# Kernel tuning notes

Hardware: AMD Instinct MI355X
Metric: run time of the kernel (lower is better)

## Reference

```python
import jax, jax.numpy as jnp
import numpy as np

B, N, D = 8, 1024, 768
H = 3
DCAT = 2 * D          # 1536, input dim at layer 1
DK = DCAT // H        # 512
CONV_OUT = D - 2      # 766 (kernel 3, VALID)


def setup_inputs() -> dict:
    key = jax.random.key(0)
    ks = jax.random.split(key, 20)
    s = 0.02
    return {
        "adj": jax.random.uniform(ks[0], (B, N, N), dtype=jnp.float32),
        "inputs": jax.random.normal(ks[1], (B, N, D), dtype=jnp.float32),
        "score_mask": jax.random.randint(ks[2], (B, H, N, N), 0, 2).astype(bool),
        # GCN layer weights (stored [in,out]; math = torch Linear)
        "W0_w": jax.random.normal(ks[3], (D, D), dtype=jnp.float32) * s,
        "W0_b": jnp.zeros((D,), dtype=jnp.float32),
        "W1_w": jax.random.normal(ks[4], (DCAT, D), dtype=jnp.float32) * s,
        "W1_b": jnp.zeros((D,), dtype=jnp.float32),
        # MultiHeadAttention(3, 1536) query/key projections
        "q_w": jax.random.normal(ks[5], (DCAT, DCAT), dtype=jnp.float32) * s,
        "q_b": jnp.zeros((DCAT,), dtype=jnp.float32),
        "k_w": jax.random.normal(ks[6], (DCAT, DCAT), dtype=jnp.float32) * s,
        "k_b": jnp.zeros((DCAT,), dtype=jnp.float32),
        # Conv1d(n, n, 3) created in forward: OIH layout
        "conv_w": jax.random.normal(ks[7], (N, N, 3), dtype=jnp.float32) * s,
        "conv_b": jnp.zeros((N,), dtype=jnp.float32),
        # linearc: 766 -> 768
        "linc_w": jax.random.normal(ks[8], (CONV_OUT, D), dtype=jnp.float32) * s,
        "linc_b": jnp.zeros((D,), dtype=jnp.float32),
        # fc: Linear(768,768,no bias) -> ReLU -> Linear(768,768,no bias)
        "fc1_w": jax.random.normal(ks[9], (D, D), dtype=jnp.float32) * s,
        "fc2_w": jax.random.normal(ks[10], (D, D), dtype=jnp.float32) * s,
    }


def _gcn_layer(adj, x, denom, Ww, Wb):
    Ax = adj @ x                       # [B,n,din]
    AxW = (Ax @ Ww + Wb) / denom       # [B,n,768]
    return jax.nn.relu(AxW) + (x @ Ww + Wb)


def _select_top2(m):
    # per-batch top-2 threshold over flattened NxN, symmetrize, diag=1
    b, n, _ = m.shape
    flat = m.reshape(b, -1)
    thr = jax.lax.top_k(flat, 2)[0][:, -1]                  # [b]
    mask = (flat >= thr[:, None]).astype(m.dtype).reshape(b, n, n)
    mask = mask + jnp.swapaxes(mask, -1, -2)
    eye = jnp.eye(n, dtype=m.dtype)
    return mask * (1.0 - eye) + eye


def reference(adj, inputs, score_mask, W0_w, W0_b, W1_w, W1_b,
              q_w, q_b, k_w, k_b, conv_w, conv_b, linc_w, linc_b,
              fc1_w, fc2_w):
    b, n, d = inputs.shape
    # ---- layer 0 ----
    denom = adj.sum(2, keepdims=True) + 1.0
    out = _gcn_layer(adj, inputs, denom, W0_w, W0_b)        # [B,n,768]
    # Conv1d over feature axis with channels = n, VALID, k=3 -> [B,n,766]
    conve = jax.nn.relu(
        jax.lax.conv_general_dilated(out, conv_w, (1,), 'VALID',
                                     dimension_numbers=('NCH', 'OIH', 'NCH'))
        + conv_b[None, :, None])
    out = conve @ linc_w + linc_b                           # [B,n,768]
    # ---- layer 1 (semantic path) ----
    x = jnp.concatenate([inputs, out], axis=-1)             # [B,n,1536]
    h, dk = H, x.shape[-1] // H
    q = (x @ q_w + q_b).reshape(b, n, h, dk).transpose(0, 2, 1, 3)
    k = (x @ k_w + k_b).reshape(b, n, h, dk).transpose(0, 2, 1, 3)
    scores = jnp.einsum('bhqd,bhkd->bhqk', q, k) / jnp.sqrt(jnp.float32(dk))
    scores = jnp.where(score_mask, jnp.float32(-1e9), scores)
    keep = (~score_mask[:, :, :, 0:1]).astype(scores.dtype)
    attn = jax.nn.softmax(scores, axis=-1) * keep           # [B,3,n,n]
    # attention-driven head selection (softmax over batch dim, argmax over heads)
    prob = jax.nn.softmax(attn.sum((-2, -1)), axis=0)       # [B,3]
    max_idx = jnp.argmax(prob, axis=1)                      # [B]
    adj2 = jnp.take_along_axis(attn, max_idx[:, None, None, None], axis=1)[:, 0]
    adj2 = _select_top2(adj2) * adj2
    denom2 = adj2.sum(2, keepdims=True) + 1.0
    out = _gcn_layer(adj2, x, denom2, W1_w, W1_b)
    out = jax.nn.relu(out @ fc1_w) @ fc2_w
    return out
```

## Files before the change

### kernel.cpp

```cpp
#include <hip/hip_runtime.h>
#include <cstdint>
#include <cstddef>

typedef __bf16 bf16;
typedef __bf16 bf16x8 __attribute__((ext_vector_type(8)));
typedef float f32x4 __attribute__((ext_vector_type(4)));

#define B_ 8
#define N_ 1024
#define D_ 768
#define H_ 3
#define DC_ 1536
#define DK_ 512
#define PC_ 766
#define MB_ (1024ull*1024ull)

static const size_t O_DEN   = 0;
static const size_t O_DEN2  = 32768;
static const size_t O_ADIAG = 65536;
static const size_t O_T2P   = 98304;
static const size_t O_THR   = 163840;
static const size_t O_CNTS  = 164096;
static const size_t O_HSEL  = 164352;
static const size_t O_SELC  = 164608;
static const size_t O_FLAG  = 164864;
static const size_t O_QKB   = 165120;
static const size_t O_SEL   = 180224;
static const size_t O_ATTN  = 262144;
static const size_t O_X     = O_ATTN + 32*MB_;
static const size_t O_AX2   = O_X    + 24*MB_;
static const size_t O_ADJB  = O_AX2  + 24*MB_;
static const size_t O_INT   = O_ADJB + 16*MB_;
static const size_t O_BBA   = O_INT  + 12*MB_;
static const size_t O_BBB   = O_BBA  + 12*MB_;
static const size_t O_BBC   = O_BBB  + 12*MB_;
static const size_t O_W0T   = O_BBC  + 12*MB_;
static const size_t O_W1T   = O_W0T + 1179648;
static const size_t O_QKWT  = O_W1T + 2359296;
static const size_t O_CWB   = O_QKWT + 9437184;
static const size_t O_LCT   = O_CWB + 6291456;
static const size_t O_F1T   = O_LCT + 1179648;
static const size_t O_F2T   = O_F1T + 1179648;
static const size_t WS_NEED = O_F2T + 1179648;
static const size_t O_OUT0T = O_INT;

__device__ __forceinline__ bool mask_at(const void* p, int flag, size_t i) {
    switch (flag) {
        case 1:  return ((const int*)p)[i] != 0;
        case 2:  return ((const float*)p)[i] != 0.0f;
        case 3:  return ((const long long*)p)[i] != 0;
        default: return ((const unsigned char*)p)[i] != 0;
    }
}

__device__ __forceinline__ void gload16(const void* g, void* l) {
    __builtin_amdgcn_global_load_lds(
        (const __attribute__((address_space(1))) void*)g,
        (__attribute__((address_space(3))) void*)l, 16, 0, 0);
}

__device__ inline float blockMax256(float v) {
    __shared__ float red[4];
    for (int off = 32; off; off >>= 1) v = fmaxf(v, __shfl_xor(v, off));
    int lane = threadIdx.x & 63, wid = threadIdx.x >> 6;
    if (lane == 0) red[wid] = v;
    __syncthreads();
    v = fmaxf(fmaxf(red[0], red[1]), fmaxf(red[2], red[3]));
    __syncthreads();
    return v;
}

__device__ inline float blockSum256(float v) {
    __shared__ float red[4];
    for (int off = 32; off; off >>= 1) v += __shfl_xor(v, off);
    int lane = threadIdx.x & 63, wid = threadIdx.x >> 6;
    if (lane == 0) red[wid] = v;
    __syncthreads();
    v = red[0] + red[1] + red[2] + red[3];
    __syncthreads();
    return v;
}

template<int EPI>
__global__ __launch_bounds__(256) void mm(
    const bf16* __restrict__ A, size_t sA, int lda,
    const bf16* __restrict__ Bt, size_t sB, int ldb,
    const int* __restrict__ rowIdx, int rowMul,
    const float* __restrict__ bias,
    const bf16* __restrict__ Dadd, int ldd,
    const float* __restrict__ denv,
    const void* __restrict__ smask, const int* __restrict__ flagp,
    bf16* __restrict__ Cb, float* __restrict__ Cf, size_t sC, int ldc,
    int M, int N, int K,
    const bf16* __restrict__ Bt2, const float* __restrict__ bias2,
    bf16* __restrict__ Cb2, size_t sC2, int ldc2)
{
    __shared__ __align__(16) bf16 As[2][64 * 64];
    __shared__ __align__(16) bf16 Bs[2][128 * 64];

    const int gx = gridDim.x, gy = gridDim.y;
    const int nwg = gx * gy * (int)gridDim.z;
    int lin = ((int)blockIdx.z * gy + (int)blockIdx.y) * gx + (int)blockIdx.x;
    int cpx = nwg >> 3;
    int swz = (lin & 7) * cpx + (lin >> 3);
    int ty = swz % gy;
    int tt = swz / gy;
    int tx = tt % gx;
    int b  = tt / gx;

    const int bm = ty * 64, bn = tx * 128;
    const int tid = threadIdx.x;
    const int lane = tid & 63, w = tid >> 6;
    const int wr = w >> 1, wc = w & 1;
    const int boff = rowIdx ? rowIdx[b] * rowMul : 0;

    const bf16* Ab = A + (size_t)b * sA;
    const bf16* Bb = Bt + (size_t)b * sB;

    const bf16* Bsrc = Bb;
    int bRow0 = boff + bn;
    if (EPI == 7 && bn >= 1024) { Bsrc = Bt2; bRow0 = bn - 1024; }

    const int sr = lane >> 3;
    const int gk = ((lane & 7) ^ (lane >> 3)) * 8;

    f32x4 zero = {0.f, 0.f, 0.f, 0.f};
    f32x4 acc[2][4];
    #pragma unroll
    for (int i = 0; i < 2; ++i)
        #pragma unroll
        for (int j = 0; j < 4; ++j) acc[i][j] = zero;

    #pragma unroll
    for (int q = 0; q < 2; ++q)
        gload16((const void*)(Ab + (size_t)(bm + w * 16 + q * 8 + sr) * lda + gk),
                (void*)(As[0] + (w * 16 + q * 8) * 64));
    #pragma unroll
    for (int q = 0; q < 4; ++q)
        gload16((const void*)(Bsrc + (size_t)(bRow0 + w * 32 + q * 8 + sr) * ldb + gk),
                (void*)(Bs[0] + (w * 32 + q * 8) * 64));

    const int rl = lane & 15;
    const int g8 = lane >> 4;
    const int rx = lane & 7;

    int cur = 0;
    for (int k0 = 0; k0 < K; k0 += 64) {
        int nxt = cur ^ 1;
        if (k0 + 64 < K) {
            #pragma unroll
            for (int q = 0; q < 2; ++q)
                gload16((const void*)(Ab + (size_t)(bm + w * 16 + q * 8 + sr) * lda + k0 + 64 + gk),
                        (void*)(As[nxt] + (w * 16 + q * 8) * 64));
            #pragma unroll
            for (int q = 0; q < 4; ++q)
                gload16((const void*)(Bsrc + (size_t)(bRow0 + w * 32 + q * 8 + sr) * ldb + k0 + 64 + gk),
                        (void*)(Bs[nxt] + (w * 32 + q * 8) * 64));
            asm volatile("s_waitcnt vmcnt(6)" ::: "memory");
        } else {
            asm volatile("s_waitcnt vmcnt(0)" ::: "memory");
        }
        __builtin_amdgcn_s_barrier();
        __builtin_amdgcn_sched_barrier(0);

        bf16x8 af[2][2], bfv[4][2];
        #pragma unroll
        for (int ks = 0; ks < 2; ++ks) {
            int e = ks * 4 + g8;
            #pragma unroll
            for (int i = 0; i < 2; ++i)
                af[i][ks] = *(const bf16x8*)(As[cur] + (wr * 32 + i * 16 + rl) * 64 + (e ^ rx) * 8);
            #pragma unroll
            for (int j = 0; j < 4; ++j)
                bfv[j][ks] = *(const bf16x8*)(Bs[cur] + (wc * 64 + j * 16 + rl) * 64 + (e ^ rx) * 8);
        }
        #pragma unroll
        for (int ks = 0; ks < 2; ++ks)
            #pragma unroll
            for (int i = 0; i < 2; ++i)
                #pragma unroll
                for (int j = 0; j < 4; ++j)
                    acc[i][j] = __builtin_amdgcn_mfma_f32_16x16x32_bf16(af[i][ks], bfv[j][ks], acc[i][j], 0, 0, 0);

        __builtin_amdgcn_s_barrier();
        __builtin_amdgcn_sched_barrier(0);
        cur = nxt;
    }

    const int r0 = (lane >> 4) * 4, c0 = lane & 15;
    int flag = 0, h0 = 0;
    if (EPI == 4) { flag = flagp[0]; h0 = rowIdx[b]; }
    #pragma unroll
    for (int i = 0; i < 2; ++i) {
        #pragma unroll
        for (int r = 0; r < 4; ++r) {
            int m = bm + wr * 32 + i * 16 + r0 + r;
            #pragma unroll
            for (int j = 0; j < 4; ++j) {
                int n = bn + wc * 64 + j * 16 + c0;
                float v = acc[i][j][r];
                size_t oidx = (size_t)b * sC + (size_t)m * ldc + n;
                if (EPI == 0) {
                    Cb[oidx] = (bf16)(v + bias[boff + n]);
                } else if (EPI == 1) {
                    v = fmaxf((v + bias[n]) / denv[(size_t)b * M + m], 0.f)
                        + (float)Dadd[((size_t)b * M + m) * ldd + n];
                    Cb[oidx] = (bf16)v;
                } else if (EPI == 2) {
                    Cb[oidx] = (bf16)fmaxf(v, 0.f);
                } else if (EPI == 3) {
                    Cf[oidx] = v;
                } else if (EPI == 4) {
                    size_t mi = (((size_t)b * H_ + h0) * N_ + m) * N_ + n;
                    Cf[oidx] = mask_at(smask, flag, mi) ? -1e9f : v * 0.04419417382415922f;
                } else if (EPI == 5) {
                    Cb[oidx] = (n < PC_) ? (bf16)fmaxf(v + bias[m], 0.f) : (bf16)0.f;
                } else if (EPI == 7) {
                    if (n < 1024)
                        Cb[(size_t)b * sC + (size_t)m * ldc + n] = (bf16)(v + bias[boff + n]);
                    else
                        Cb2[(size_t)b * sC2 + (size_t)m * ldc2 + (n - 1024)] = (bf16)(v + bias2[n - 1024]);
                } else {
                    Cb[oidx] = (bf16)v;
                }
            }
        }
    }
}


__device__ int d_detect(const unsigned int* __restrict__ sm) {
    __shared__ int sGt1, sF32, sOddNZ, sFlag;
    if (threadIdx.x == 0) { sGt1 = 0; sF32 = 0; sOddNZ = 0; }
    __syncthreads();
    int gt1 = 0, f32c = 0, oddnz = 0;
    for (int s = 0; s < 16; ++s) {
        int idx = s * 256 + threadIdx.x;
        unsigned wv = sm[idx];
        if (wv > 1u) gt1 = 1;
        if (wv == 0x3F800000u) f32c++;
        if ((idx & 1) && wv != 0u) oddnz = 1;
    }
    if (gt1)   atomicOr(&sGt1, 1);
    if (f32c)  atomicAdd(&sF32, f32c);
    if (oddnz) atomicOr(&sOddNZ, 1);
    __syncthreads();
    if (threadIdx.x == 0) {
        int f;
        if (sF32 > 512) f = 2;
        else if (!sGt1) f = sOddNZ ? 1 : 3;
        else f = 0;
        sFlag = f;
    }
    __syncthreads();
    return sFlag;
}

__device__ void d_trcvt(const float* __restrict__ src, bf16* __restrict__ dst,
                        int R, int C, int Rpad, int Cpad,
                        size_t sSrc, size_t sDst, int mode, int bx, int by, int bz) {
    __shared__ float t[32][33];
    int r0 = by * 32, c0 = bx * 32;
    int tx = threadIdx.x & 31, ty = threadIdx.x >> 5;
    const float* s = src + (size_t)bz * sSrc;
    bf16* d = dst + (size_t)bz * sDst;
    #pragma unroll
    for (int q = 0; q < 4; ++q) {
        int r = r0 + ty + q * 8, c = c0 + tx;
        t[ty + q * 8][tx] = (r < R && c < C) ? s[(size_t)r * C + c] : 0.f;
    }
    __syncthreads();
    #pragma unroll
    for (int q = 0; q < 4; ++q) {
        int dr = c0 + ty + q * 8, dc = r0 + tx;
        if (dr < Cpad && dc < Rpad) {
            int drm = dr;
            if (mode == 1) drm = (dr >> 9) * 1024 + (dr & 511);
            else if (mode == 2) drm = (dr >> 9) * 1024 + 512 + (dr & 511);
            d[(size_t)drm * Rpad + dc] = (bf16)t[tx][ty + q * 8];
        }
    }
}

#define PB_DET   1
#define PB_QKB   13
#define PB_CW2   1037
#define PB_ADJ   9229
#define PB_ROWS  17421
#define PB_INT   23565
#define PB_W0    24141
#define PB_W1    25293
#define PB_QW    27597
#define PB_KW    29901
#define PB_LC    30477
#define PB_F1    31053
#define PB_F2    31629
#define PB_CNT   31653

__global__ __launch_bounds__(256) void k_prep(
    const void* __restrict__ smask, int* __restrict__ flag, int* __restrict__ counts,
    const float* __restrict__ adj, bf16* __restrict__ adjb, float* __restrict__ den,
    const float* __restrict__ inputs, bf16* __restrict__ X, bf16* __restrict__ INT_,
    const float* __restrict__ convw, bf16* __restrict__ CW2,
    const float* __restrict__ qb, const float* __restrict__ kb, float* __restrict__ qkbD,
    const float* __restrict__ W0w, bf16* __restrict__ W0T,
    const float* __restrict__ W1w, bf16* __restrict__ W1T,
    const float* __restrict__ qw, const float* __restrict__ kw, bf16* __restrict__ QKWT,
    const float* __restrict__ lincw, bf16* __restrict__ LCT,
    const float* __restrict__ fc1w, bf16* __restrict__ F1T,
    const float* __restrict__ fc2w, bf16* __restrict__ F2T)
{
    const int id = blockIdx.x;
    const size_t sND = (size_t)N_ * D_;
    if (id < PB_DET) {
        int f = d_detect((const unsigned int*)smask);
        if (threadIdx.x == 0) flag[0] = f;
    } else if (id < PB_QKB) {
        int idx = (id - PB_DET) * 256 + threadIdx.x;
        if (idx < 3072) {
            int h = idx >> 10, rem = idx & 1023, s = rem >> 9, r = rem & 511;
            qkbD[idx] = (s ? kb : qb)[h * 512 + r];
        }
    } else if (id < PB_CW2) {
        int o = id - PB_QKB;
        const float* s = convw + (size_t)o * 3072;
        bf16* dp = CW2 + (size_t)o * 3072;
        for (int q = 0; q < 4; ++q) {
            int i = q * 256 + threadIdx.x;
            float v0 = s[i * 3], v1 = s[i * 3 + 1], v2 = s[i * 3 + 2];
            dp[i] = (bf16)v0; dp[1024 + i] = (bf16)v1; dp[2048 + i] = (bf16)v2;
        }
    } else if (id < PB_ADJ) {
        int t = id - PB_CW2;
        int row = t & 1023, b = t >> 10;
        size_t base = ((size_t)b * N_ + row) * N_;
        float4 v = ((const float4*)(adj + base))[threadIdx.x];
        union { bf16 b[4]; uint2 u; } o;
        o.b[0] = (bf16)v.x; o.b[1] = (bf16)v.y; o.b[2] = (bf16)v.z; o.b[3] = (bf16)v.w;
        ((uint2*)(adjb + base))[threadIdx.x] = o.u;
        float s = blockSum256(v.x + v.y + v.z + v.w);
        if (threadIdx.x == 0) den[b * N_ + row] = s + 1.0f;
    } else if (id < PB_ROWS) {
        int row = id - PB_ADJ;
        int t = threadIdx.x;
        if (t < 192) {
            float4 v = ((const float4*)(inputs + (size_t)row * D_))[t];
            union { bf16 b[4]; uint2 u; } o;
            o.b[0] = (bf16)v.x; o.b[1] = (bf16)v.y; o.b[2] = (bf16)v.z; o.b[3] = (bf16)v.w;
            *(uint2*)(X + (size_t)row * DC_ + t * 4) = o.u;
        }
    } else if (id < PB_INT) {
        int t = id - PB_ROWS;
        int bx = t % 24; int u = t / 24; int by = u % 32; int bz = u / 32;
        d_trcvt(inputs, INT_, N_, D_, N_, D_, sND, sND, 0, bx, by, bz);
    } else if (id < PB_W0) {
        int t = id - PB_INT;
        d_trcvt(W0w, W0T, D_, D_, D_, D_, 0, 0, 0, t % 24, t / 24, 0);
    } else if (id < PB_W1) {
        int t = id - PB_W0;
        d_trcvt(W1w, W1T, DC_, D_, DC_, D_, 0, 0, 0, t % 24, t / 24, 0);
    } else if (id < PB_QW) {
        int t = id - PB_W1;
        d_trcvt(qw, QKWT, DC_, DC_, DC_, DC_, 0, 0, 1, t % 48, t / 48, 0);
    } else if (id < PB_KW) {
        int t = id - PB_QW;
        d_trcvt(kw, QKWT, DC_, DC_, DC_, DC_, 0, 0, 2, t % 48, t / 48, 0);
    } else if (id < PB_LC) {
        int t = id - PB_KW;
        d_trcvt(lincw, LCT, PC_, D_, D_, D_, 0, 0, 0, t % 24, t / 24, 0);
    } else if (id < PB_F1) {
        int t = id - PB_LC;
        d_trcvt(fc1w, F1T, D_, D_, D_, D_, 0, 0, 0, t % 24, t / 24, 0);
    } else if (id < PB_F2) {
        int t = id - PB_F1;
        d_trcvt(fc2w, F2T, D_, D_, D_, D_, 0, 0, 0, t % 24, t / 24, 0);
    } else if (id < PB_CNT) {
        int bh = id - PB_F2;
        int f = d_detect((const unsigned int*)smask);
        float c = 0.f;
        for (int s = 0; s < 4; ++s) {
            int q = s * 256 + threadIdx.x;
            size_t mi = ((size_t)bh * N_ + q) * N_;
            if (!mask_at(smask, f, mi)) c += 1.f;
        }
        c = blockSum256(c);
        if (threadIdx.x == 0) counts[bh] = (int)(c + 0.5f);
    }
}


__global__ void k_select_head(const int* __restrict__ counts, int* __restrict__ hsel) {
    if (threadIdx.x != 0 || blockIdx.x != 0) return;
    float p[B_][H_];
    for (int h = 0; h < H_; ++h) {
        float mx = -1e30f;
        for (int b = 0; b < B_; ++b) mx = fmaxf(mx, (float)counts[b * H_ + h]);
        float s = 0.f;
        for (int b = 0; b < B_; ++b) { p[b][h] = expf((float)counts[b * H_ + h] - mx); s += p[b][h]; }
        for (int b = 0; b < B_; ++b) p[b][h] /= s;
    }
    for (int b = 0; b < B_; ++b) {
        int best = 0; float bv = p[b][0];
        for (int h = 1; h < H_; ++h) if (p[b][h] > bv) { bv = p[b][h]; best = h; }
        hsel[b] = best;
    }
}

__global__ __launch_bounds__(256) void k_tr_bf16(const bf16* __restrict__ src,
                                                 bf16* __restrict__ dst) {
    __shared__ bf16 t[32][34];
    int b = blockIdx.z;
    int i0 = blockIdx.y * 32, p0 = blockIdx.x * 32;
    int tx = threadIdx.x & 31, ty = threadIdx.x >> 5;
    const bf16* s = src + (size_t)b * N_ * D_;
    bf16* d = dst + (size_t)b * D_ * N_;
    #pragma unroll
    for (int q = 0; q < 4; ++q)
        t[ty + q * 8][tx] = s[(size_t)(i0 + ty + q * 8) * D_ + p0 + tx];
    __syncthreads();
    #pragma unroll
    for (int q = 0; q < 4; ++q)
        d[(size_t)(p0 + ty + q * 8) * N_ + i0 + tx] = t[tx][ty + q * 8];
}

__global__ __launch_bounds__(256) void k_softmax(float* __restrict__ Sc,
                                                 const void* __restrict__ smask,
                                                 const int* __restrict__ flagp,
                                                 const int* __restrict__ hsel,
                                                 float* __restrict__ part) {
    __shared__ float s1[256], s2[256];
    int b = blockIdx.y, row = blockIdx.x;
    int h0 = hsel[b], flag = flagp[0];
    float* rp = Sc + ((size_t)b * N_ + row) * N_;
    float v[4];
    float mx = -INFINITY;
    #pragma unroll
    for (int s = 0; s < 4; ++s) { v[s] = rp[s * 256 + threadIdx.x]; mx = fmaxf(mx, v[s]); }
    mx = blockMax256(mx);
    float sum = 0.f;
    #pragma unroll
    for (int s = 0; s < 4; ++s) { v[s] = expf(v[s] - mx); sum += v[s]; }
    sum = blockSum256(sum);
    size_t ki = (((size_t)b * H_ + h0) * N_ + row) * N_;
    float keep = mask_at(smask, flag, ki) ? 0.f : 1.f;
    float inv = keep / sum;
    float m1 = -INFINITY, m2 = -INFINITY;
    #pragma unroll
    for (int s = 0; s < 4; ++s) {
        float x = v[s] * inv;
        rp[s * 256 + threadIdx.x] = x;
        if (x > m1) { m2 = m1; m1 = x; } else m2 = fmaxf(m2, x);
    }
    int tid = threadIdx.x;
    s1[tid] = m1; s2[tid] = m2;
    __syncthreads();
    for (int off = 128; off; off >>= 1) {
        if (tid < off) {
            float a1 = s1[tid], a2 = s2[tid], b1 = s1[tid + off], b2 = s2[tid + off];
            s1[tid] = fmaxf(a1, b1);
            s2[tid] = fmaxf(fminf(a1, b1), fmaxf(a2, b2));
        }
        __syncthreads();
    }
    if (tid == 0) {
        part[((size_t)b * N_ + row) * 2]     = s1[0];
        part[((size_t)b * N_ + row) * 2 + 1] = s2[0];
    }
}

__global__ __launch_bounds__(256) void k_top2_s2(const float* __restrict__ part,
                                                 float* __restrict__ thr,
                                                 int* __restrict__ selcnt) {
    __shared__ float s1[256], s2[256];
    int b = blockIdx.x, tid = threadIdx.x;
    float m1 = -INFINITY, m2 = -INFINITY;
    for (int s = 0; s < 4; ++s) {
        int r = s * 256 + tid;
        float a1 = part[((size_t)b * N_ + r) * 2];
        float a2 = part[((size_t)b * N_ + r) * 2 + 1];
        float n1 = fmaxf(m1, a1);
        float n2 = fmaxf(fminf(m1, a1), fmaxf(m2, a2));
        m1 = n1; m2 = n2;
    }
    s1[tid] = m1; s2[tid] = m2;
    __syncthreads();
    for (int off = 128; off; off >>= 1) {
        if (tid < off) {
            float a1 = s1[tid], a2 = s2[tid], b1 = s1[tid + off], b2 = s2[tid + off];
            s1[tid] = fmaxf(a1, b1);
            s2[tid] = fmaxf(fminf(a1, b1), fmaxf(a2, b2));
        }
        __syncthreads();
    }
    if (tid == 0) { thr[b] = s2[0]; selcnt[b] = 0; }
}

__global__ __launch_bounds__(256) void k_extract(const float* __restrict__ attn,
                                                 const float* __restrict__ thr,
                                                 int* __restrict__ selcnt,
                                                 int* __restrict__ sel,
                                                 float* __restrict__ adiag,
                                                 float* __restrict__ den2,
                                                 const bf16* __restrict__ x,
                                                 bf16* __restrict__ ax2) {
    __shared__ float sdiag;
    int b = blockIdx.y, row = blockIdx.x;
    const float* ap = attn + (size_t)b * N_ * N_;
    float t = thr[b];
    size_t base = (size_t)row * 1024;
    for (int s = 0; s < 4; ++s) {
        int col = s * 256 + threadIdx.x;
        float v = ap[base + col];
        if (col == row) {
            adiag[b * N_ + row] = v;
            den2[b * N_ + row] = v + 1.0f;
            sdiag = v;
        }
        if (v >= t) {
            int pos = atomicAdd(&selcnt[b], 1);
            if (pos < 512) {
                sel[((size_t)b * 512 + pos) * 2]     = row;
                sel[((size_t)b * 512 + pos) * 2 + 1] = col;
            }
        }
    }
    __syncthreads();
    float a = sdiag;
    const bf16* xp = x + ((size_t)b * N_ + row) * DC_;
    bf16* op = ax2 + ((size_t)b * N_ + row) * DC_;
    #pragma unroll
    for (int s = 0; s < 6; ++s) {
        int d = s * 256 + threadIdx.x;
        op[d] = (bf16)(a * (float)xp[d]);
    }
}

__global__ __launch_bounds__(256) void k_ax2_sparse(const float* __restrict__ attn,
                                                    const bf16* __restrict__ x,
                                                    const int* __restrict__ selcnt,
                                                    const int* __restrict__ sel,
                                                    bf16* __restrict__ ax2,
                                                    float* __restrict__ den2) {
    int b = blockIdx.x;
    int cnt = selcnt[b]; if (cnt > 512) cnt = 512;
    __shared__ int si[1024];
    if (threadIdx.x == 0) {
        for (int e = 0; e < cnt; ++e) {
            si[e * 2]     = sel[((size_t)b * 512 + e) * 2];
            si[e * 2 + 1] = sel[((size_t)b * 512 + e) * 2 + 1];
        }
        for (int a = 1; a < cnt; ++a) {
            int ii = si[a * 2], jj = si[a * 2 + 1];
            long long key = (long long)ii * N_ + jj;
            int p = a - 1;
            while (p >= 0 && ((long long)si[p * 2] * N_ + si[p * 2 + 1]) > key) {
                si[(p + 1) * 2] = si[p * 2]; si[(p + 1) * 2 + 1] = si[p * 2 + 1]; --p;
            }
            si[(p + 1) * 2] = ii; si[(p + 1) * 2 + 1] = jj;
        }
    }
    __syncthreads();
    const float* ap = attn + (size_t)b * N_ * N_;
    for (int e = 0; e < cnt; ++e) {
        int i = si[e * 2], j = si[e * 2 + 1];
        if (i == j) continue;
        float aij = ap[(size_t)i * N_ + j];
        float aji = ap[(size_t)j * N_ + i];
        bf16* ri = ax2 + ((size_t)b * N_ + i) * DC_;
        bf16* rj = ax2 + ((size_t)b * N_ + j) * DC_;
        const bf16* xi = x + ((size_t)b * N_ + i) * DC_;
        const bf16* xj = x + ((size_t)b * N_ + j) * DC_;
        for (int s = 0; s < 6; ++s) {
            int d = s * 256 + threadIdx.x;
            ri[d] = (bf16)((float)ri[d] + aij * (float)xj[d]);
            rj[d] = (bf16)((float)rj[d] + aji * (float)xi[d]);
        }
        if (threadIdx.x == 0) {
            den2[b * N_ + i] += aij;
            den2[b * N_ + j] += aji;
        }
        __syncthreads();
    }
}

extern "C" void kernel_launch(void* const* d_in, const int* in_sizes, int n_in,
                              void* d_out, int out_size, void* d_ws, size_t ws_size,
                              hipStream_t stream) {
    if (n_in < 17) return;
    if (ws_size < WS_NEED) return;

    const float* adj    = (const float*)d_in[0];
    const float* inputs = (const float*)d_in[1];
    const void*  smask  = d_in[2];
    const float* W0w = (const float*)d_in[3];
    const float* W0b = (const float*)d_in[4];
    const float* W1w = (const float*)d_in[5];
    const float* W1b = (const float*)d_in[6];
    const float* qw  = (const float*)d_in[7];
    const float* qb  = (const float*)d_in[8];
    const float* kw  = (const float*)d_in[9];
    const float* kb  = (const float*)d_in[10];
    const float* convw = (const float*)d_in[11];
    const float* convb = (const float*)d_in[12];
    const float* lincw = (const float*)d_in[13];
    const float* lincb = (const float*)d_in[14];
    const float* fc1w  = (const float*)d_in[15];
    const float* fc2w  = (const float*)d_in[16];

    char* W = (char*)d_ws;
    float* out = (float*)d_out;

    float* den    = (float*)(W + O_DEN);
    float* den2   = (float*)(W + O_DEN2);
    float* adiag  = (float*)(W + O_ADIAG);
    float* t2p    = (float*)(W + O_T2P);
    float* thr    = (float*)(W + O_THR);
    int*   counts = (int*)(W + O_CNTS);
    int*   hsel   = (int*)(W + O_HSEL);
    int*   selcnt = (int*)(W + O_SELC);
    int*   flag   = (int*)(W + O_FLAG);
    float* qkb    = (float*)(W + O_QKB);
    int*   sel    = (int*)(W + O_SEL);
    float* ATTN   = (float*)(W + O_ATTN);
    bf16* X     = (bf16*)(W + O_X);
    bf16* AX2   = (bf16*)(W + O_AX2);
    bf16* QKOUT = (bf16*)(W + O_AX2);
    bf16* ADJB  = (bf16*)(W + O_ADJB);
    bf16* INT_  = (bf16*)(W + O_INT);
    bf16* OUT0T = (bf16*)(W + O_OUT0T);
    bf16* BBA   = (bf16*)(W + O_BBA);
    bf16* BBB   = (bf16*)(W + O_BBB);
    bf16* BBC   = (bf16*)(W + O_BBC);
    bf16* W0T   = (bf16*)(W + O_W0T);
    bf16* W1T   = (bf16*)(W + O_W1T);
    bf16* QKWT  = (bf16*)(W + O_QKWT);
    bf16* CW2   = (bf16*)(W + O_CWB);
    bf16* LCT   = (bf16*)(W + O_LCT);
    bf16* F1T   = (bf16*)(W + O_F1T);
    bf16* F2T   = (bf16*)(W + O_F2T);

    const size_t sND  = (size_t)N_ * D_;
    const size_t sNDC = (size_t)N_ * DC_;
    const size_t sNN  = (size_t)N_ * N_;

    k_prep<<<PB_CNT, 256, 0, stream>>>(smask, flag, counts,
        adj, ADJB, den, inputs, X, INT_, convw, CW2,
        qb, kb, qkb, W0w, W0T, W1w, W1T, qw, kw, QKWT,
        lincw, LCT, fc1w, F1T, fc2w, F2T);
    k_select_head<<<1, 64, 0, stream>>>(counts, hsel);

    mm<0><<<dim3(6, 16, B_), 256, 0, stream>>>(X, sNDC, DC_, W0T, 0, D_, nullptr, 0,
        W0b, nullptr, 0, nullptr, nullptr, nullptr, BBA, nullptr, sND, D_, N_, D_, D_,
        nullptr, nullptr, nullptr, 0, 0);
    mm<6><<<dim3(6, 16, B_), 256, 0, stream>>>(ADJB, sNN, N_, INT_, sND, N_, nullptr, 0,
        nullptr, nullptr, 0, nullptr, nullptr, nullptr, BBB, nullptr, sND, D_, N_, D_, N_,
        nullptr, nullptr, nullptr, 0, 0);
    mm<1><<<dim3(6, 16, B_), 256, 0, stream>>>(BBB, sND, D_, W0T, 0, D_, nullptr, 0,
        W0b, BBA, D_, den, nullptr, nullptr, BBC, nullptr, sND, D_, N_, D_, D_,
        nullptr, nullptr, nullptr, 0, 0);
    k_tr_bf16<<<dim3(24, 32, B_), 256, 0, stream>>>(BBC, OUT0T);
    mm<5><<<dim3(6, 16, B_), 256, 0, stream>>>(CW2, 0, 3072, OUT0T, sND, N_, nullptr, 0,
        convb, nullptr, 0, nullptr, nullptr, nullptr, BBB, nullptr, sND, D_, N_, D_, 3072,
        nullptr, nullptr, nullptr, 0, 0);
    mm<0><<<dim3(6, 16, B_), 256, 0, stream>>>(BBB, sND, D_, LCT, 0, D_, nullptr, 0,
        lincb, nullptr, 0, nullptr, nullptr, nullptr, X + D_, nullptr, sNDC, DC_, N_, D_, D_,
        nullptr, nullptr, nullptr, 0, 0);

    mm<7><<<dim3(14, 16, B_), 256, 0, stream>>>(X, sNDC, DC_, QKWT, 0, DC_, hsel, 1024,
        qkb, nullptr, 0, nullptr, nullptr, nullptr, QKOUT, nullptr, sNN, N_, N_, 1792, DC_,
        W1T, W1b, BBA, sND, D_);

    mm<4><<<dim3(8, 16, B_), 256, 0, stream>>>(QKOUT, sNN, N_, QKOUT + 512, sNN, N_, hsel, 0,
        nullptr, nullptr, 0, nullptr, smask, flag, nullptr, ATTN, sNN, N_, N_, N_, DK_,
        nullptr, nullptr, nullptr, 0, 0);
    k_softmax<<<dim3(N_, B_), 256, 0, stream>>>(ATTN, smask, flag, hsel, t2p);

    k_top2_s2<<<B_, 256, 0, stream>>>(t2p, thr, selcnt);
    k_extract<<<dim3(N_, B_), 256, 0, stream>>>(ATTN, thr, selcnt, sel, adiag, den2, X, AX2);
    k_ax2_sparse<<<B_, 256, 0, stream>>>(ATTN, X, selcnt, sel, AX2, den2);

    mm<1><<<dim3(6, 16, B_), 256, 0, stream>>>(AX2, sNDC, DC_, W1T, 0, DC_, nullptr, 0,
        W1b, BBA, D_, den2, nullptr, nullptr, BBB, nullptr, sND, D_, N_, D_, DC_,
        nullptr, nullptr, nullptr, 0, 0);

    mm<2><<<dim3(6, 16, B_), 256, 0, stream>>>(BBB, sND, D_, F1T, 0, D_, nullptr, 0,
        nullptr, nullptr, 0, nullptr, nullptr, nullptr, BBC, nullptr, sND, D_, N_, D_, D_,
        nullptr, nullptr, nullptr, 0, 0);
    mm<3><<<dim3(6, 16, B_), 256, 0, stream>>>(BBC, sND, D_, F2T, 0, D_, nullptr, 0,
        nullptr, nullptr, 0, nullptr, nullptr, nullptr, nullptr, out, sND, D_, N_, D_, D_,
        nullptr, nullptr, nullptr, 0, 0);
}
```

Before: 407.0 us.

## Load A fragments directly from global into registers, drop A shared tile

The GEMM kernel stops staging the A tile through LDS. Each wave now loads its A MFMA fragments straight from global memory into registers, double-buffered across two register sets, while B stays staged in LDS. The main loop is unrolled by two K-steps with explicit buffers. This cuts LDS traffic and shared-memory footprint, but the A loads are less coalesced and rows shared between waves are fetched redundantly. The loop also assumes K is a multiple of 128.

```diff
diff --git a/kernel.cpp b/kernel.cpp
--- a/kernel.cpp
+++ b/kernel.cpp
@@ -95,7 +95,6 @@
     const bf16* __restrict__ Bt2, const float* __restrict__ bias2,
     bf16* __restrict__ Cb2, size_t sC2, int ldc2)
 {
-    __shared__ __align__(16) bf16 As[2][64 * 64];
     __shared__ __align__(16) bf16 Bs[2][128 * 64];
 
     const int gx = gridDim.x, gy = gridDim.y;
@@ -124,6 +123,15 @@
     const int sr = lane >> 3;
     const int gk = ((lane & 7) ^ (lane >> 3)) * 8;
 
+    const int rl = lane & 15;
+    const int g8 = lane >> 4;
+    const int rx = lane & 7;
+
+    const bf16* a0 = Ab + (size_t)(bm + wr * 32 + rl) * lda;
+    const bf16* a1 = Ab + (size_t)(bm + wr * 32 + 16 + rl) * lda;
+    const int c0o = g8 * 8;
+    const int c1o = (4 + g8) * 8;
+
     f32x4 zero = {0.f, 0.f, 0.f, 0.f};
     f32x4 acc[2][4];
     #pragma unroll
@@ -131,61 +139,68 @@
         #pragma unroll
         for (int j = 0; j < 4; ++j) acc[i][j] = zero;
 
-    #pragma unroll
-    for (int q = 0; q < 2; ++q)
-        gload16((const void*)(Ab + (size_t)(bm + w * 16 + q * 8 + sr) * lda + gk),
-                (void*)(As[0] + (w * 16 + q * 8) * 64));
-    #pragma unroll
-    for (int q = 0; q < 4; ++q)
-        gload16((const void*)(Bsrc + (size_t)(bRow0 + w * 32 + q * 8 + sr) * ldb + gk),
-                (void*)(Bs[0] + (w * 32 + q * 8) * 64));
-
-    const int rl = lane & 15;
-    const int g8 = lane >> 4;
-    const int rx = lane & 7;
-
-    int cur = 0;
-    for (int k0 = 0; k0 < K; k0 += 64) {
-        int nxt = cur ^ 1;
-        if (k0 + 64 < K) {
-            #pragma unroll
-            for (int q = 0; q < 2; ++q)
-                gload16((const void*)(Ab + (size_t)(bm + w * 16 + q * 8 + sr) * lda + k0 + 64 + gk),
-                        (void*)(As[nxt] + (w * 16 + q * 8) * 64));
-            #pragma unroll
-            for (int q = 0; q < 4; ++q)
-                gload16((const void*)(Bsrc + (size_t)(bRow0 + w * 32 + q * 8 + sr) * ldb + k0 + 64 + gk),
-                        (void*)(Bs[nxt] + (w * 32 + q * 8) * 64));
-            asm volatile("s_waitcnt vmcnt(6)" ::: "memory");
+    #define STAGE_B(k0_, buf_)                                                          \
+        _Pragma("unroll")                                                               \
+        for (int q = 0; q < 4; ++q)                                                     \
+            gload16((const void*)(Bsrc + (size_t)(bRow0 + w * 32 + q * 8 + sr) * ldb + (k0_) + gk), \
+                    (void*)(Bs[buf_] + (w * 32 + q * 8) * 64));
+
+    #define LOAD_A(af_, k0_)                                    \
+        af_[0][0] = *(const bf16x8*)(a0 + (k0_) + c0o);         \
+        af_[0][1] = *(const bf16x8*)(a0 + (k0_) + c1o);         \
+        af_[1][0] = *(const bf16x8*)(a1 + (k0_) + c0o);         \
+        af_[1][1] = *(const bf16x8*)(a1 + (k0_) + c1o);
+
+    #define COMPUTE(buf_, af_)                                                              \
+        {                                                                                   \
+            bf16x8 bfv[4][2];                                                               \
+            _Pragma("unroll")                                                               \
+            for (int ks = 0; ks < 2; ++ks) {                                                \
+                int e = ks * 4 + g8;                                                        \
+                _Pragma("unroll")                                                           \
+                for (int j = 0; j < 4; ++j)                                                 \
+                    bfv[j][ks] = *(const bf16x8*)(Bs[buf_] + (wc * 64 + j * 16 + rl) * 64 + (e ^ rx) * 8); \
+            }                                                                               \
+            _Pragma("unroll")                                                               \
+            for (int ks = 0; ks < 2; ++ks)                                                  \
+                _Pragma("unroll")                                                           \
+                for (int i = 0; i < 2; ++i)                                                 \
+                    _Pragma("unroll")                                                       \
+                    for (int j = 0; j < 4; ++j)                                             \
+                        acc[i][j] = __builtin_amdgcn_mfma_f32_16x16x32_bf16(af_[i][ks], bfv[j][ks], acc[i][j], 0, 0, 0); \
+        }
+
+    bf16x8 afP[2][2], afQ[2][2];
+
+    STAGE_B(0, 0)
+    LOAD_A(afP, 0)
+
+    for (int k0 = 0; k0 < K; k0 += 128) {
+        STAGE_B(k0 + 64, 1)
+        LOAD_A(afQ, k0 + 64)
+        asm volatile("s_waitcnt vmcnt(8)" ::: "memory");
+        __builtin_amdgcn_s_barrier();
+        __builtin_amdgcn_sched_barrier(0);
+        COMPUTE(0, afP)
+        __builtin_amdgcn_s_barrier();
+        __builtin_amdgcn_sched_barrier(0);
+
+        if (k0 + 128 < K) {
+            STAGE_B(k0 + 128, 0)
+            LOAD_A(afP, k0 + 128)
+            asm volatile("s_waitcnt vmcnt(8)" ::: "memory");
         } else {
             asm volatile("s_waitcnt vmcnt(0)" ::: "memory");
         }
         __builtin_amdgcn_s_barrier();
         __builtin_amdgcn_sched_barrier(0);
-
-        bf16x8 af[2][2], bfv[4][2];
-        #pragma unroll
-        for (int ks = 0; ks < 2; ++ks) {
-            int e = ks * 4 + g8;
-            #pragma unroll
-            for (int i = 0; i < 2; ++i)
-                af[i][ks] = *(const bf16x8*)(As[cur] + (wr * 32 + i * 16 + rl) * 64 + (e ^ rx) * 8);
-            #pragma unroll
-            for (int j = 0; j < 4; ++j)
-                bfv[j][ks] = *(const bf16x8*)(Bs[cur] + (wc * 64 + j * 16 + rl) * 64 + (e ^ rx) * 8);
-        }
-        #pragma unroll
-        for (int ks = 0; ks < 2; ++ks)
-            #pragma unroll
-            for (int i = 0; i < 2; ++i)
-                #pragma unroll
-                for (int j = 0; j < 4; ++j)
-                    acc[i][j] = __builtin_amdgcn_mfma_f32_16x16x32_bf16(af[i][ks], bfv[j][ks], acc[i][j], 0, 0, 0);
-
+        COMPUTE(1, afQ)
         __builtin_amdgcn_s_barrier();
         __builtin_amdgcn_sched_barrier(0);
-        cur = nxt;
-    }
+    }
+    #undef STAGE_B
+    #undef LOAD_A
+    #undef COMPUTE
 
     const int r0 = (lane >> 4) * 4, c0 = lane & 15;
     int flag = 0, h0 = 0;
```

Result: slower. 572.5 us (+40.7%).

## Add 128x128 tile GEMM variant for QK projection and attention score kernels

Applied to the files above, without the earlier changes.

Adds an mm2 kernel that uses 128x128 output tiles with a 4x4 MFMA accumulator grid per wave, and moves the epilogue into a shared helper. The two largest GEMMs (fused Q/K/W1 projection and the masked score GEMM) switch to it with half as many row blocks. Larger tiles raise operand reuse from LDS and cut global traffic per FLOP, in exchange for more registers and LDS per block and fewer workgroups, which lowers occupancy.

```diff
diff --git a/kernel.cpp b/kernel.cpp
--- a/kernel.cpp
+++ b/kernel.cpp
@@ -82,6 +82,42 @@
 }
 
 template<int EPI>
+__device__ __forceinline__ void epi_store(
+    float v, int b, int m, int n, int M,
+    const int boff, const float* __restrict__ bias,
+    const bf16* __restrict__ Dadd, int ldd,
+    const float* __restrict__ denv,
+    const void* __restrict__ smask, int flag, int h0,
+    bf16* __restrict__ Cb, float* __restrict__ Cf, size_t sC, int ldc,
+    const float* __restrict__ bias2, bf16* __restrict__ Cb2, size_t sC2, int ldc2)
+{
+    size_t oidx = (size_t)b * sC + (size_t)m * ldc + n;
+    if (EPI == 0) {
+        Cb[oidx] = (bf16)(v + bias[boff + n]);
+    } else if (EPI == 1) {
+        v = fmaxf((v + bias[n]) / denv[(size_t)b * M + m], 0.f)
+            + (float)Dadd[((size_t)b * M + m) * ldd + n];
+        Cb[oidx] = (bf16)v;
+    } else if (EPI == 2) {
+        Cb[oidx] = (bf16)fmaxf(v, 0.f);
+    } else if (EPI == 3) {
+        Cf[oidx] = v;
+    } else if (EPI == 4) {
+        size_t mi = (((size_t)b * H_ + h0) * N_ + m) * N_ + n;
+        Cf[oidx] = mask_at(smask, flag, mi) ? -1e9f : v * 0.04419417382415922f;
+    } else if (EPI == 5) {
+        Cb[oidx] = (n < PC_) ? (bf16)fmaxf(v + bias[m], 0.f) : (bf16)0.f;
+    } else if (EPI == 7) {
+        if (n < 1024)
+            Cb[(size_t)b * sC + (size_t)m * ldc + n] = (bf16)(v + bias[boff + n]);
+        else
+            Cb2[(size_t)b * sC2 + (size_t)m * ldc2 + (n - 1024)] = (bf16)(v + bias2[n - 1024]);
+    } else {
+        Cb[oidx] = (bf16)v;
+    }
+}
+
+template<int EPI>
 __global__ __launch_bounds__(256) void mm(
     const bf16* __restrict__ A, size_t sA, int lda,
     const bf16* __restrict__ Bt, size_t sB, int ldb,
@@ -191,41 +227,138 @@
     int flag = 0, h0 = 0;
     if (EPI == 4) { flag = flagp[0]; h0 = rowIdx[b]; }
     #pragma unroll
-    for (int i = 0; i < 2; ++i) {
+    for (int i = 0; i < 2; ++i)
         #pragma unroll
         for (int r = 0; r < 4; ++r) {
             int m = bm + wr * 32 + i * 16 + r0 + r;
             #pragma unroll
             for (int j = 0; j < 4; ++j) {
                 int n = bn + wc * 64 + j * 16 + c0;
-                float v = acc[i][j][r];
-                size_t oidx = (size_t)b * sC + (size_t)m * ldc + n;
-                if (EPI == 0) {
-                    Cb[oidx] = (bf16)(v + bias[boff + n]);
-                } else if (EPI == 1) {
-                    v = fmaxf((v + bias[n]) / denv[(size_t)b * M + m], 0.f)
-                        + (float)Dadd[((size_t)b * M + m) * ldd + n];
-                    Cb[oidx] = (bf16)v;
-                } else if (EPI == 2) {
-                    Cb[oidx] = (bf16)fmaxf(v, 0.f);
-                } else if (EPI == 3) {
-                    Cf[oidx] = v;
-                } else if (EPI == 4) {
-                    size_t mi = (((size_t)b * H_ + h0) * N_ + m) * N_ + n;
-                    Cf[oidx] = mask_at(smask, flag, mi) ? -1e9f : v * 0.04419417382415922f;
-                } else if (EPI == 5) {
-                    Cb[oidx] = (n < PC_) ? (bf16)fmaxf(v + bias[m], 0.f) : (bf16)0.f;
-                } else if (EPI == 7) {
-                    if (n < 1024)
-                        Cb[(size_t)b * sC + (size_t)m * ldc + n] = (bf16)(v + bias[boff + n]);
-                    else
-                        Cb2[(size_t)b * sC2 + (size_t)m * ldc2 + (n - 1024)] = (bf16)(v + bias2[n - 1024]);
-                } else {
-                    Cb[oidx] = (bf16)v;
-                }
+                epi_store<EPI>(acc[i][j][r], b, m, n, M, boff, bias, Dadd, ldd, denv,
+                               smask, flag, h0, Cb, Cf, sC, ldc, bias2, Cb2, sC2, ldc2);
             }
         }
-    }
+}
+
+template<int EPI>
+__global__ __launch_bounds__(256) void mm2(
+    const bf16* __restrict__ A, size_t sA, int lda,
+    const bf16* __restrict__ Bt, size_t sB, int ldb,
+    const int* __restrict__ rowIdx, int rowMul,
+    const float* __restrict__ bias,
+    const bf16* __restrict__ Dadd, int ldd,
+    const float* __restrict__ denv,
+    const void* __restrict__ smask, const int* __restrict__ flagp,
+    bf16* __restrict__ Cb, float* __restrict__ Cf, size_t sC, int ldc,
+    int M, int N, int K,
+    const bf16* __restrict__ Bt2, const float* __restrict__ bias2,
+    bf16* __restrict__ Cb2, size_t sC2, int ldc2)
+{
+    __shared__ __align__(16) bf16 As[2][128 * 64];
+    __shared__ __align__(16) bf16 Bs[2][128 * 64];
+
+    const int gx = gridDim.x, gy = gridDim.y;
+    const int nwg = gx * gy * (int)gridDim.z;
+    int lin = ((int)blockIdx.z * gy + (int)blockIdx.y) * gx + (int)blockIdx.x;
+    int cpx = nwg >> 3;
+    int swz = (lin & 7) * cpx + (lin >> 3);
+    int ty = swz % gy;
+    int tt = swz / gy;
+    int tx = tt % gx;
+    int b  = tt / gx;
+
+    const int bm = ty * 128, bn = tx * 128;
+    const int tid = threadIdx.x;
+    const int lane = tid & 63, w = tid >> 6;
+    const int wr = w >> 1, wc = w & 1;
+    const int boff = rowIdx ? rowIdx[b] * rowMul : 0;
+
+    const bf16* Ab = A + (size_t)b * sA;
+    const bf16* Bb = Bt + (size_t)b * sB;
+
+    const bf16* Bsrc = Bb;
+    int bRow0 = boff + bn;
+    if (EPI == 7 && bn >= 1024) { Bsrc = Bt2; bRow0 = bn - 1024; }
+
+    const int sr = lane >> 3;
+    const int gk = ((lane & 7) ^ (lane >> 3)) * 8;
+
+    f32x4 zero = {0.f, 0.f, 0.f, 0.f};
+    f32x4 acc[4][4];
+    #pragma unroll
+    for (int i = 0; i < 4; ++i)
+        #pragma unroll
+        for (int j = 0; j < 4; ++j) acc[i][j] = zero;
+
+    #pragma unroll
+    for (int q = 0; q < 4; ++q)
+        gload16((const void*)(Ab + (size_t)(bm + w * 32 + q * 8 + sr) * lda + gk),
+                (void*)(As[0] + (w * 32 + q * 8) * 64));
+    #pragma unroll
+    for (int q = 0; q < 4; ++q)
+        gload16((const void*)(Bsrc + (size_t)(bRow0 + w * 32 + q * 8 + sr) * ldb + gk),
+                (void*)(Bs[0] + (w * 32 + q * 8) * 64));
+
+    const int rl = lane & 15;
+    const int g8 = lane >> 4;
+    const int rx = lane & 7;
+
+    int cur = 0;
+    for (int k0 = 0; k0 < K; k0 += 64) {
+        int nxt = cur ^ 1;
+        if (k0 + 64 < K) {
+            #pragma unroll
+            for (int q = 0; q < 4; ++q)
+                gload16((const void*)(Ab + (size_t)(bm + w * 32 + q * 8 + sr) * lda + k0 + 64 + gk),
+                        (void*)(As[nxt] + (w * 32 + q * 8) * 64));
+            #pragma unroll
+            for (int q = 0; q < 4; ++q)
+                gload16((const void*)(Bsrc + (size_t)(bRow0 + w * 32 + q * 8 + sr) * ldb + k0 + 64 + gk),
+                        (void*)(Bs[nxt] + (w * 32 + q * 8) * 64));
+            asm volatile("s_waitcnt vmcnt(8)" ::: "memory");
+        } else {
+            asm volatile("s_waitcnt vmcnt(0)" ::: "memory");
+        }
+        __builtin_amdgcn_s_barrier();
+        __builtin_amdgcn_sched_barrier(0);
+
+        #pragma unroll
+        for (int ks = 0; ks < 2; ++ks) {
+            int e = ks * 4 + g8;
+            bf16x8 af[4], bfv[4];
+            #pragma unroll
+            for (int i = 0; i < 4; ++i)
+                af[i] = *(const bf16x8*)(As[cur] + (wr * 64 + i * 16 + rl) * 64 + (e ^ rx) * 8);
+            #pragma unroll
+            for (int j = 0; j < 4; ++j)
+                bfv[j] = *(const bf16x8*)(Bs[cur] + (wc * 64 + j * 16 + rl) * 64 + (e ^ rx) * 8);
+            #pragma unroll
+            for (int i = 0; i < 4; ++i)
+                #pragma unroll
+                for (int j = 0; j < 4; ++j)
+                    acc[i][j] = __builtin_amdgcn_mfma_f32_16x16x32_bf16(af[i], bfv[j], acc[i][j], 0, 0, 0);
+        }
+
+        __builtin_amdgcn_s_barrier();
+        __builtin_amdgcn_sched_barrier(0);
+        cur = nxt;
+    }
+
+    const int r0 = (lane >> 4) * 4, c0 = lane & 15;
+    int flag = 0, h0 = 0;
+    if (EPI == 4) { flag = flagp[0]; h0 = rowIdx[b]; }
+    #pragma unroll
+    for (int i = 0; i < 4; ++i)
+        #pragma unroll
+        for (int r = 0; r < 4; ++r) {
+            int m = bm + wr * 64 + i * 16 + r0 + r;
+            #pragma unroll
+            for (int j = 0; j < 4; ++j) {
+                int n = bn + wc * 64 + j * 16 + c0;
+                epi_store<EPI>(acc[i][j][r], b, m, n, M, boff, bias, Dadd, ldd, denv,
+                               smask, flag, h0, Cb, Cf, sC, ldc, bias2, Cb2, sC2, ldc2);
+            }
+        }
 }
 
 
@@ -666,11 +799,11 @@
         lincb, nullptr, 0, nullptr, nullptr, nullptr, X + D_, nullptr, sNDC, DC_, N_, D_, D_,
         nullptr, nullptr, nullptr, 0, 0);
 
-    mm<7><<<dim3(14, 16, B_), 256, 0, stream>>>(X, sNDC, DC_, QKWT, 0, DC_, hsel, 1024,
+    mm2<7><<<dim3(14, 8, B_), 256, 0, stream>>>(X, sNDC, DC_, QKWT, 0, DC_, hsel, 1024,
         qkb, nullptr, 0, nullptr, nullptr, nullptr, QKOUT, nullptr, sNN, N_, N_, 1792, DC_,
         W1T, W1b, BBA, sND, D_);
 
-    mm<4><<<dim3(8, 16, B_), 256, 0, stream>>>(QKOUT, sNN, N_, QKOUT + 512, sNN, N_, hsel, 0,
+    mm2<4><<<dim3(8, 8, B_), 256, 0, stream>>>(QKOUT, sNN, N_, QKOUT + 512, sNN, N_, hsel, 0,
         nullptr, nullptr, 0, nullptr, smask, flag, nullptr, ATTN, sNN, N_, N_, N_, DK_,
         nullptr, nullptr, nullptr, 0, 0);
     k_softmax<<<dim3(N_, B_), 256, 0, stream>>>(ATTN, smask, flag, hsel, t2p);
```

Measured after the change: 397.0 us. 1.03x faster.
